# Kernel tuning notes

Hardware: AMD Instinct MI355X
Metric: run time of the kernel (lower is better)

Reference implementation:

```python
import jax, jax.numpy as jnp
import numpy as np

B, S, DM, H, DFF, NL = 4, 1024, 512, 8, 2048, 2
D = DM // H
EPS = 1e-9


def setup_inputs() -> dict:
    key = jax.random.key(0)
    ks = jax.random.split(key, 16)
    x = jax.random.normal(ks[0], (B, S, DM), jnp.float32)
    # padding-style mask: 1.0 where attention is blocked
    pad = (jax.random.uniform(ks[1], (B, S)) < 0.1).astype(jnp.float32)
    mask = jnp.maximum(pad[:, :, None], pad[:, None, :])  # [B,S,S]
    protok = jax.random.randint(ks[2], (B, S), 0, 21).astype(jnp.int32)

    def w(k, fan_in, fan_out):
        lim = np.sqrt(6.0 / (fan_in + fan_out)).astype(np.float32)
        return jax.random.uniform(k, (fan_in, fan_out), jnp.float32, -lim, lim)

    return {
        "x": x, "mask": mask, "protok": protok,
        "wq": w(ks[3], DM, DM), "bq": jnp.zeros((DM,), jnp.float32),
        "wk": w(ks[4], DM, DM), "bk": jnp.zeros((DM,), jnp.float32),
        "wv": w(ks[5], DM, DM), "bv": jnp.zeros((DM,), jnp.float32),
        "wo": w(ks[6], DM, DM), "bo": jnp.zeros((DM,), jnp.float32),
        "w1": w(ks[7], DM, DFF), "b1": jnp.zeros((DFF,), jnp.float32),
        "w2": w(ks[8], DFF, DM), "b2": jnp.zeros((DM,), jnp.float32),
        "ln1_g": jnp.ones((DM,), jnp.float32), "ln1_b": jnp.zeros((DM,), jnp.float32),
        "ln2_g": jnp.ones((DM,), jnp.float32), "ln2_b": jnp.zeros((DM,), jnp.float32),
        "layer_num": NL,
    }


def _layernorm(y, g, b):
    m = jnp.mean(y, axis=-1, keepdims=True)
    v = jnp.mean(jnp.square(y - m), axis=-1, keepdims=True)
    return (y - m) * jax.lax.rsqrt(v + EPS) * g + b


def reference(x, mask, protok, wq, bq, wk, bk, wv, bv, wo, bo,
              w1, b1, w2, b2, ln1_g, ln1_b, ln2_g, ln2_b, layer_num):
    b, s, dm = x.shape
    # count_nonzero(protok[0:1,:]) rescale for the 2D softmax (seq == max_pro_len)
    nz = jnp.count_nonzero(protok[0]).astype(jnp.float32)
    neg = mask[:, None, :, :] * -1e9  # [B,1,S,S] broadcast over heads

    def split(t):  # [B,S,DM] -> [B,H,S,D]
        return t.reshape(b, s, H, D).transpose(0, 2, 1, 3)

    def layer(h):
        q = split(h @ wq + bq)
        k = split(h @ wk + bk)
        v = split(h @ wv + bv)
        logits = jnp.einsum('bhid,bhjd->bhij', q, k) / jnp.sqrt(jnp.float32(D))
        logits = logits + neg
        # 2D softmax jointly over axes (2,3), then rescale by nonzero-token count
        A = jax.nn.softmax(logits.reshape(b, H, s * s), axis=-1).reshape(b, H, s, s) * nz
        # faithful quirk: output = A^T @ v
        o = jnp.einsum('bhji,bhjd->bhid', A, v)
        o = o.transpose(0, 2, 1, 3).reshape(b, s, dm)
        attn_out = o @ wo + bo
        out1 = _layernorm(h + attn_out, ln1_g, ln1_b)
        ffn = jax.nn.relu(out1 @ w1 + b1) @ w2 + b2
        return _layernorm(out1 + ffn, ln2_g, ln2_b)

    # Encoders reuses one shared layer layer_num times (self.rencoder overwritten in loop)
    for _ in range(int(layer_num)):
        x = layer(x)
    return x
```

## Files before the change

kernel.cpp:

```cpp
#include <hip/hip_runtime.h>

typedef unsigned short u16;
typedef __bf16 bf16x8 __attribute__((ext_vector_type(8)));
typedef float f32x4 __attribute__((ext_vector_type(4)));
typedef unsigned int u32x4 __attribute__((ext_vector_type(4)));
typedef u16 u16x4 __attribute__((ext_vector_type(4)));

#define LOG2E 1.44269504089f
#define SOFF 16.0f

__device__ __forceinline__ f32x4 mfma16(bf16x8 a, bf16x8 b, f32x4 c) {
    return __builtin_amdgcn_mfma_f32_16x16x32_bf16(a, b, c, 0, 0, 0);
}
__device__ __forceinline__ u16 f2bf(float f) {
    union { float f; unsigned u; } x; x.f = f;
    unsigned r = x.u + 0x7FFFu + ((x.u >> 16) & 1u);
    return (u16)(r >> 16);
}
__device__ __forceinline__ float bf2f(u16 u) {
    union { unsigned u; float f; } x; x.u = ((unsigned)u) << 16;
    return x.f;
}
__device__ __forceinline__ void gload_lds16(const u16* g, u16* l) {
    __builtin_amdgcn_global_load_lds((const __attribute__((address_space(1))) unsigned int*)g,
                                     (__attribute__((address_space(3))) unsigned int*)l, 16, 0, 0);
}

__device__ __forceinline__ void transp_tile(const float* __restrict__ in, u16* __restrict__ out,
                                            int R, int C, int r0, int c0,
                                            float (*t)[33], int tid) {
    const int tx = tid & 31, ty = tid >> 5;
#pragma unroll
    for (int k = 0; k < 4; ++k) t[ty + k * 8][tx] = in[(size_t)(r0 + ty + k * 8) * C + c0 + tx];
    __syncthreads();
#pragma unroll
    for (int k = 0; k < 4; ++k) out[(size_t)(c0 + ty + k * 8) * R + r0 + tx] = f2bf(t[tx][ty + k * 8]);
}

__global__ __launch_bounds__(256) void prep_kernel(
    const float* __restrict__ x,
    const float* __restrict__ wq, const float* __restrict__ wk,
    const float* __restrict__ wv, const float* __restrict__ wo,
    const float* __restrict__ w1, const float* __restrict__ w2,
    const float* __restrict__ mask, const int* __restrict__ protok,
    u16* __restrict__ hbf, u16* __restrict__ wqT, u16* __restrict__ wkT,
    u16* __restrict__ wvT, u16* __restrict__ woT, u16* __restrict__ w1T, u16* __restrict__ w2T,
    float* __restrict__ padneg, float* __restrict__ nzf) {
    __shared__ float t[32][33];
    __shared__ int red[256];
    const int id = blockIdx.x, tid = threadIdx.x;
    if (id < 1024) {
        const int z = id >> 8, rem = id & 255;
        const float* in = z == 0 ? wq : (z == 1 ? wk : (z == 2 ? wv : wo));
        u16* out = z == 0 ? wqT : (z == 1 ? wkT : (z == 2 ? wvT : woT));
        transp_tile(in, out, 512, 512, (rem >> 4) * 32, (rem & 15) * 32, t, tid);
    } else if (id < 2048) {
        const int rem = id - 1024;
        transp_tile(w1, w1T, 512, 2048, (rem >> 6) * 32, (rem & 63) * 32, t, tid);
    } else if (id < 3072) {
        const int rem = id - 2048;
        transp_tile(w2, w2T, 2048, 512, (rem >> 4) * 32, (rem & 15) * 32, t, tid);
    } else if (id < 4096) {
        const int i = ((id - 3072) * 256 + tid) * 8;
        f32x4 a = *(const f32x4*)(x + i);
        f32x4 b = *(const f32x4*)(x + i + 4);
        u16x4 o0, o1;
#pragma unroll
        for (int k = 0; k < 4; ++k) { o0[k] = f2bf(a[k]); o1[k] = f2bf(b[k]); }
        *(u16x4*)(hbf + i) = o0;
        *(u16x4*)(hbf + i + 4) = o1;
    } else if (id == 4096) {
        for (int i = tid; i < 4096; i += 256) {
            const int b = i >> 10, s = i & 1023;
            const float m = mask[(size_t)((b << 10) + s) * 1024 + s];
            padneg[i] = (m > 0.5f) ? -1.5e9f : -SOFF;
        }
    } else {
        int c = 0;
        for (int i = tid; i < 1024; i += 256) c += (protok[i] != 0) ? 1 : 0;
        red[tid] = c;
        __syncthreads();
        for (int s = 128; s > 0; s >>= 1) {
            if (tid < s) red[tid] += red[tid + s];
            __syncthreads();
        }
        if (tid == 0) nzf[0] = (float)red[0];
    }
}

template <int BM, int BN, int MODE>
__global__ __launch_bounds__(256) void gemm_bf16(
    const u16* __restrict__ A,
    const u16* __restrict__ Bt0, const u16* __restrict__ Bt1, const u16* __restrict__ Bt2,
    const float* __restrict__ bias0, const float* __restrict__ bias1, const float* __restrict__ bias2,
    void* __restrict__ dst0, void* __restrict__ dst1, void* __restrict__ dst2,
    const int K, const int N) {
    constexpr int BK = 64;
    constexpr int WM = BM / 2, WN = BN / 2, MI = WM / 16, NI = WN / 16;
    __shared__ u16 lA[BM * BK];
    __shared__ u16 lB[BN * BK];
    const int tid = threadIdx.x;
    const int w = tid >> 6, lane = tid & 63, q = lane >> 4, ln = lane & 15;
    const int wm = w >> 1, wn = w & 1;
    const int id = blockIdx.y * gridDim.x + blockIdx.x;
    const int mper = gridDim.y >> 3;
    const int rest = id >> 3;
    const int by = (id & 7) * mper + (rest % mper);
    const int bx = rest / mper;
    const int n0 = bx * BN, m0 = by * BM;
    const int rr = lane >> 3;
    const int cs = ((lane & 7) ^ rr) * 8;

    const u16* Bt;
    const float* bias;
    int nb, sel = 0;
    if (MODE == 0) {
        sel = n0 >> 9;
        Bt = sel == 0 ? Bt0 : (sel == 1 ? Bt1 : Bt2);
        bias = sel == 0 ? bias0 : (sel == 1 ? bias1 : bias2);
        nb = n0 & 511;
    } else {
        Bt = Bt0; bias = bias0; nb = n0;
    }

    const f32x4 vzero = {0.f, 0.f, 0.f, 0.f};
    f32x4 acc[MI][NI];
#pragma unroll
    for (int i = 0; i < MI; ++i)
#pragma unroll
        for (int j = 0; j < NI; ++j) acc[i][j] = vzero;

    const int swa = ln & 7;
    for (int k0 = 0; k0 < K; k0 += BK) {
        const u16* Ag = A + (size_t)m0 * K + k0;
        const u16* Bg = Bt + (size_t)nb * K + k0;
#pragma unroll
        for (int c = 0; c < BM / 32; ++c) {
            const int r = (w * (BM / 32) + c) * 8;
            gload_lds16(Ag + (size_t)(r + rr) * K + cs, &lA[r * BK]);
        }
#pragma unroll
        for (int c = 0; c < BN / 32; ++c) {
            const int r = (w * (BN / 32) + c) * 8;
            gload_lds16(Bg + (size_t)(r + rr) * K + cs, &lB[r * BK]);
        }
        __syncthreads();
#pragma unroll
        for (int kb = 0; kb < 2; ++kb) {
            bf16x8 af[MI], bfr[NI];
#pragma unroll
            for (int mi = 0; mi < MI; ++mi)
                af[mi] = *(const bf16x8*)&lA[(wm * WM + mi * 16 + ln) * BK + ((((kb << 2) + q) ^ swa) << 3)];
#pragma unroll
            for (int ni = 0; ni < NI; ++ni)
                bfr[ni] = *(const bf16x8*)&lB[(wn * WN + ni * 16 + ln) * BK + ((((kb << 2) + q) ^ swa) << 3)];
#pragma unroll
            for (int mi = 0; mi < MI; ++mi)
#pragma unroll
                for (int ni = 0; ni < NI; ++ni) acc[mi][ni] = mfma16(af[mi], bfr[ni], acc[mi][ni]);
        }
        __syncthreads();
    }

    const float scl = (MODE == 0 && sel == 1) ? 0.125f * LOG2E : 1.0f;
#pragma unroll
    for (int mi = 0; mi < MI; ++mi) {
#pragma unroll
        for (int ni = 0; ni < NI; ++ni) {
            const int col = n0 + wn * WN + ni * 16 + ln;
            const float bv = bias[MODE == 0 ? (col & 511) : col];
#pragma unroll
            for (int r = 0; r < 4; ++r) {
                const int row = m0 + wm * WM + mi * 16 + q * 4 + r;
                const float v = (acc[mi][ni][r] + bv) * scl;
                if (MODE == 0) {
                    const int cc = col & 511, hh = cc >> 6, dd = cc & 63;
                    const int bb = row >> 10, ss = row & 1023;
                    if (sel < 2) {
                        u16* dq = (u16*)(sel == 0 ? dst0 : dst1);
                        dq[(((bb << 3) + hh) * 1024 + ss) * 64 + dd] = f2bf(v);
                    } else {
                        ((u16*)dst2)[(((bb << 3) + hh) * 64 + dd) * 1024 + ss] = f2bf(v);
                    }
                } else if (MODE == 1) {
                    ((float*)dst0)[(size_t)row * N + col] = v;
                } else {
                    ((u16*)dst0)[(size_t)row * N + col] = f2bf(fmaxf(v, 0.f));
                }
            }
        }
    }
}

__global__ __launch_bounds__(256) void gemm_wo(
    const u16* __restrict__ Ounc, const float* __restrict__ blkZ, const float* __restrict__ nzf,
    const u16* __restrict__ Bt, const float* __restrict__ bias,
    float* __restrict__ dst) {
    constexpr int BM = 64, BN = 64, BK = 64, N = 512;
    constexpr int WM = 32, WN = 32, MI = 2, NI = 2;
    __shared__ u16 lA[BM * BK];
    __shared__ u16 lB[BN * BK];
    __shared__ float facsh[8];
    const int tid = threadIdx.x;
    const int w = tid >> 6, lane = tid & 63, q = lane >> 4, ln = lane & 15;
    const int wm = w >> 1, wn = w & 1;
    const int id = blockIdx.y * gridDim.x + blockIdx.x;
    const int mper = gridDim.y >> 3;
    const int rest = id >> 3;
    const int by = (id & 7) * mper + (rest % mper);
    const int bx = rest / mper;
    const int n0 = bx * BN, m0 = by * BM;
    const int b = m0 >> 10, mi0 = m0 & 1023;
    const int rr = lane >> 3;
    const int cs = ((lane & 7) ^ rr) * 8;

    {
        const int h = tid >> 5, sub = tid & 31;
        float v = blkZ[((sub >> 3) << 8) + ((b << 3) + h) * 8 + (sub & 7)];
#pragma unroll
        for (int o = 1; o < 32; o <<= 1) v += __shfl_xor(v, o);
        if (sub == 0) facsh[h] = nzf[0] / v;
    }
    __syncthreads();

    const f32x4 vzero = {0.f, 0.f, 0.f, 0.f};
    f32x4 acc[MI][NI];
#pragma unroll
    for (int i = 0; i < MI; ++i)
#pragma unroll
        for (int j = 0; j < NI; ++j) acc[i][j] = vzero;

    const int ra = tid >> 2;
    const int dseg = (tid & 3) * 16;
    const int swa = ln & 7;
    for (int k0 = 0; k0 < 512; k0 += BK) {
        const int h = k0 >> 6;
        const float fac = facsh[h];
        {
            const size_t gi = (size_t)(((b << 3) + h) << 10) + mi0 + ra;
            float vals[16];
#pragma unroll
            for (int k = 0; k < 16; ++k) vals[k] = 0.f;
#pragma unroll
            for (int c = 0; c < 4; ++c) {
                const u16* src = Ounc + (((size_t)c) << 21) + gi * 64 + dseg;
                bf16x8 x0 = *(const bf16x8*)src;
                bf16x8 x1 = *(const bf16x8*)(src + 8);
#pragma unroll
                for (int k = 0; k < 8; ++k) { vals[k] += (float)x0[k]; vals[k + 8] += (float)x1[k]; }
            }
            u16 tmp[16];
#pragma unroll
            for (int k = 0; k < 16; ++k) tmp[k] = f2bf(vals[k] * fac);
            const int c0 = (tid & 3) * 2;
            *(u32x4*)&lA[ra * BK + ((c0 ^ (ra & 7)) << 3)] = *(u32x4*)&tmp[0];
            *(u32x4*)&lA[ra * BK + (((c0 + 1) ^ (ra & 7)) << 3)] = *(u32x4*)&tmp[8];
        }
        const u16* Bg = Bt + (size_t)n0 * 512 + k0;
#pragma unroll
        for (int c = 0; c < BN / 32; ++c) {
            const int r = (w * (BN / 32) + c) * 8;
            gload_lds16(Bg + (size_t)(r + rr) * 512 + cs, &lB[r * BK]);
        }
        __syncthreads();
#pragma unroll
        for (int kb = 0; kb < 2; ++kb) {
            bf16x8 af[MI], bfr[NI];
#pragma unroll
            for (int mi = 0; mi < MI; ++mi)
                af[mi] = *(const bf16x8*)&lA[(wm * WM + mi * 16 + ln) * BK + ((((kb << 2) + q) ^ swa) << 3)];
#pragma unroll
            for (int ni = 0; ni < NI; ++ni)
                bfr[ni] = *(const bf16x8*)&lB[(wn * WN + ni * 16 + ln) * BK + ((((kb << 2) + q) ^ swa) << 3)];
#pragma unroll
            for (int mi = 0; mi < MI; ++mi)
#pragma unroll
                for (int ni = 0; ni < NI; ++ni) acc[mi][ni] = mfma16(af[mi], bfr[ni], acc[mi][ni]);
        }
        __syncthreads();
    }

#pragma unroll
    for (int mi = 0; mi < MI; ++mi) {
#pragma unroll
        for (int ni = 0; ni < NI; ++ni) {
            const int col = n0 + wn * WN + ni * 16 + ln;
            const float bv = bias[col];
#pragma unroll
            for (int r = 0; r < 4; ++r) {
                const int row = m0 + wm * WM + mi * 16 + q * 4 + r;
                dst[(size_t)row * N + col] = acc[mi][ni][r] + bv;
            }
        }
    }
}

#define PSTR 68
__global__ __launch_bounds__(256) void flash_kernel(
    const u16* __restrict__ Kb, const u16* __restrict__ Qb, const u16* __restrict__ VT,
    const float* __restrict__ padneg,
    u16* __restrict__ Ounc, float* __restrict__ blkZ) {
    __shared__ u16 ldsQ[64 * 64];
    __shared__ u16 ldsV[64 * 64];
    __shared__ u16 P[4][16 * PSTR];
    __shared__ float zred[4];
    const int blk = blockIdx.x, ck = blockIdx.y;
    const int ig = blk & 7, bh = blk >> 3, b = bh >> 3;
    const int i0 = ig << 7;
    const int tid = threadIdx.x;
    const int w = tid >> 6, lane = tid & 63, q = lane >> 4, ln = lane & 15;

    bf16x8 af[2][2];
    float pi[2][4];
    const float* pn = padneg + (b << 10);
#pragma unroll
    for (int it = 0; it < 2; ++it) {
        const u16* Ka = Kb + ((bh << 10) + i0 + (it << 6) + (w << 4) + ln) * 64;
        af[it][0] = *(const bf16x8*)(Ka + q * 8);
        af[it][1] = *(const bf16x8*)(Ka + 32 + q * 8);
#pragma unroll
        for (int r = 0; r < 4; ++r) pi[it][r] = pn[i0 + (it << 6) + (w << 4) + (q << 2) + r];
    }
    const u16* Qbase = Qb + (bh << 10) * 64;
    const u16* Vbase = VT + (bh << 6) * 1024;

    float lsum[2][4] = {{0.f, 0.f, 0.f, 0.f}, {0.f, 0.f, 0.f, 0.f}};
    const f32x4 vzero = {0.f, 0.f, 0.f, 0.f};
    f32x4 acc[2][4];
#pragma unroll
    for (int it = 0; it < 2; ++it)
#pragma unroll
        for (int ds = 0; ds < 4; ++ds) acc[it][ds] = vzero;
    u16* Pw = &P[w][0];

    const int srow = lane >> 3;
    const int scol = ((lane & 7) ^ srow) * 8;
    const int sw = ln & 7;
    const int half = w & 1;

    for (int js = 0; js < 4; ++js) {
        const int j0 = (ck << 8) + (js << 6);
        if (w < 2) {
            const u16* src = Qbase + (size_t)(j0 + half * 32) * 64;
#pragma unroll
            for (int c = 0; c < 4; ++c) {
                const int r = half * 32 + c * 8;
                gload_lds16(src + (size_t)(c * 8 + srow) * 64 + scol, &ldsQ[r * 64]);
            }
        } else {
            const u16* src = Vbase + (size_t)(half * 32) * 1024 + j0;
#pragma unroll
            for (int c = 0; c < 4; ++c) {
                const int r = half * 32 + c * 8;
                gload_lds16(src + (size_t)(c * 8 + srow) * 1024 + scol, &ldsV[r * 64]);
            }
        }
        __syncthreads();
#pragma unroll
        for (int it = 0; it < 2; ++it) {
#pragma unroll
            for (int jt = 0; jt < 4; ++jt) {
                const int jr = (jt << 4) + ln;
                const float pj = pn[j0 + jr];
                bf16x8 b0 = *(const bf16x8*)&ldsQ[jr * 64 + ((q ^ sw) << 3)];
                bf16x8 b1 = *(const bf16x8*)&ldsQ[jr * 64 + (((q + 4) ^ sw) << 3)];
                f32x4 c = vzero;
                c = mfma16(af[it][0], b0, c);
                c = mfma16(af[it][1], b1, c);
#pragma unroll
                for (int r = 0; r < 4; ++r) {
                    const float pe = exp2f(c[r] + fminf(pi[it][r], pj));
                    lsum[it][r] += pe;
                    Pw[((q << 2) + r) * PSTR + (jt << 4) + ln] = f2bf(pe);
                }
            }
            const bf16x8 pa0 = *(const bf16x8*)(Pw + ln * PSTR + q * 8);
            const bf16x8 pa1 = *(const bf16x8*)(Pw + ln * PSTR + 32 + q * 8);
#pragma unroll
            for (int ds = 0; ds < 4; ++ds) {
                const int vr = (ds << 4) + ln;
                bf16x8 v0 = *(const bf16x8*)&ldsV[vr * 64 + ((q ^ sw) << 3)];
                bf16x8 v1 = *(const bf16x8*)&ldsV[vr * 64 + (((q + 4) ^ sw) << 3)];
                acc[it][ds] = mfma16(pa0, v0, acc[it][ds]);
                acc[it][ds] = mfma16(pa1, v1, acc[it][ds]);
            }
        }
        __syncthreads();
    }
    u16* Oc = Ounc + ((size_t)ck << 21);
#pragma unroll
    for (int it = 0; it < 2; ++it) {
        const int t = (bh << 10) + i0 + (it << 6) + (w << 4) + (q << 2);
#pragma unroll
        for (int ds = 0; ds < 4; ++ds)
#pragma unroll
            for (int r = 0; r < 4; ++r) Oc[(size_t)(t + r) * 64 + (ds << 4) + ln] = f2bf(acc[it][ds][r]);
    }
    float s = (lsum[0][0] + lsum[0][1]) + (lsum[0][2] + lsum[0][3]) +
              (lsum[1][0] + lsum[1][1]) + (lsum[1][2] + lsum[1][3]);
#pragma unroll
    for (int o = 1; o < 64; o <<= 1) s += __shfl_xor(s, o);
    if (lane == 0) zred[w] = s;
    __syncthreads();
    if (tid == 0) blkZ[(ck << 8) + blk] = (zred[0] + zred[1]) + (zred[2] + zred[3]);
}

__global__ __launch_bounds__(256) void ln_kernel(
    const float* __restrict__ base, const float* __restrict__ delta,
    const float* __restrict__ g, const float* __restrict__ bb,
    float* __restrict__ of32, u16* __restrict__ obf) {
    const int t = blockIdx.x * 4 + (threadIdx.x >> 6);
    const int lane = threadIdx.x & 63;
    const int off = t * 512 + lane * 8;
    f32x4 a0 = *(const f32x4*)(base + off);
    f32x4 a1 = *(const f32x4*)(base + off + 4);
    f32x4 e0 = *(const f32x4*)(delta + off);
    f32x4 e1 = *(const f32x4*)(delta + off + 4);
    float v[8];
#pragma unroll
    for (int k = 0; k < 4; ++k) { v[k] = a0[k] + e0[k]; v[k + 4] = a1[k] + e1[k]; }
    float s = 0.f;
#pragma unroll
    for (int k = 0; k < 8; ++k) s += v[k];
#pragma unroll
    for (int o = 32; o > 0; o >>= 1) s += __shfl_xor(s, o);
    const float mean = s * (1.f / 512.f);
    float vs = 0.f;
#pragma unroll
    for (int k = 0; k < 8; ++k) { const float d = v[k] - mean; vs += d * d; }
#pragma unroll
    for (int o = 32; o > 0; o >>= 1) vs += __shfl_xor(vs, o);
    const float r = rsqrtf(vs * (1.f / 512.f) + 1e-9f);
    f32x4 y0, y1;
    u16x4 o0, o1;
#pragma unroll
    for (int k = 0; k < 4; ++k) {
        const int c = lane * 8 + k;
        const float ya = (v[k] - mean) * r * g[c] + bb[c];
        y0[k] = ya; o0[k] = f2bf(ya);
        const int c2 = c + 4;
        const float yb = (v[k + 4] - mean) * r * g[c2] + bb[c2];
        y1[k] = yb; o1[k] = f2bf(yb);
    }
    *(f32x4*)(of32 + off) = y0;
    *(f32x4*)(of32 + off + 4) = y1;
    *(u16x4*)(obf + off) = o0;
    *(u16x4*)(obf + off + 4) = o1;
}


extern "C" void kernel_launch(void* const* d_in, const int* in_sizes, int n_in,
                              void* d_out, int out_size, void* d_ws, size_t ws_size,
                              hipStream_t stream) {
    const float* x = (const float*)d_in[0];
    const float* mask = (const float*)d_in[1];
    const int* protok = (const int*)d_in[2];
    const float* wq = (const float*)d_in[3]; const float* bq = (const float*)d_in[4];
    const float* wk = (const float*)d_in[5]; const float* bk = (const float*)d_in[6];
    const float* wv = (const float*)d_in[7]; const float* bv = (const float*)d_in[8];
    const float* wo = (const float*)d_in[9]; const float* bo = (const float*)d_in[10];
    const float* w1 = (const float*)d_in[11]; const float* b1 = (const float*)d_in[12];
    const float* w2 = (const float*)d_in[13]; const float* b2 = (const float*)d_in[14];
    const float* ln1g = (const float*)d_in[15]; const float* ln1b = (const float*)d_in[16];
    const float* ln2g = (const float*)d_in[17]; const float* ln2b = (const float*)d_in[18];

    char* p = (char*)d_ws;
    auto take = [&](size_t bytes) -> char* {
        char* r = p;
        p += (bytes + 255) & ~(size_t)255;
        return r;
    };
    u16* wqT = (u16*)take(512 * 512 * 2);
    u16* wkT = (u16*)take(512 * 512 * 2);
    u16* wvT = (u16*)take(512 * 512 * 2);
    u16* woT = (u16*)take(512 * 512 * 2);
    u16* w1T = (u16*)take(2048 * 512 * 2);
    u16* w2T = (u16*)take(512 * 2048 * 2);
    u16* hbf = (u16*)take(4096 * 512 * 2);
    float* hf32 = (float*)take(4096 * 512 * 4);
    u16* qb = (u16*)take(32 * 1024 * 64 * 2);
    u16* kb = (u16*)take(32 * 1024 * 64 * 2);
    u16* vT = (u16*)take(32 * 64 * 1024 * 2);
    u16* Ounc = (u16*)take(4ull * 32 * 1024 * 64 * 2);
    float* blkZ = (float*)take(1024 * 4);
    float* nzf = (float*)take(256);
    float* padneg = (float*)take(4096 * 4);
    float* attn = (float*)take(4096 * 512 * 4);
    float* out1f = (float*)take(4096 * 512 * 4);
    u16* out1bf = (u16*)take(4096 * 512 * 2);
    u16* f1 = (u16*)take(4096 * 2048 * 2);
    float* ffn = attn;

    prep_kernel<<<dim3(4098), 256, 0, stream>>>(
        x, wq, wk, wv, wo, w1, w2, mask, protok,
        hbf, wqT, wkT, wvT, woT, w1T, w2T, padneg, nzf);

    const float* hin = x;
    for (int l = 0; l < 2; ++l) {
        gemm_bf16<128, 64, 0><<<dim3(24, 32), 256, 0, stream>>>(
            hbf, wqT, wkT, wvT, bq, bk, bv, qb, kb, vT, 512, 1536);
        flash_kernel<<<dim3(256, 4), 256, 0, stream>>>(kb, qb, vT, padneg, Ounc, blkZ);
        gemm_wo<<<dim3(8, 64), 256, 0, stream>>>(Ounc, blkZ, nzf, woT, bo, attn);
        ln_kernel<<<dim3(1024), 256, 0, stream>>>(hin, attn, ln1g, ln1b, out1f, out1bf);
        gemm_bf16<128, 128, 2><<<dim3(16, 32), 256, 0, stream>>>(
            out1bf, w1T, w1T, w1T, b1, b1, b1, f1, f1, f1, 512, 2048);
        gemm_bf16<64, 64, 1><<<dim3(8, 64), 256, 0, stream>>>(
            f1, w2T, w2T, w2T, b2, b2, b2, ffn, ffn, ffn, 2048, 512);
        float* hout = (l == 1) ? (float*)d_out : hf32;
        ln_kernel<<<dim3(1024), 256, 0, stream>>>(out1f, ffn, ln2g, ln2b, hout, hbf);
        hin = hf32;
    }
}
```

Before: 335.2 us.

## Double-buffer LDS tiles in GEMMs and flash kernel, halve attention split chunks

Adds ping-pong shared-memory buffers to the generic GEMM, the Wo GEMM and the flash attention kernel, so global-to-LDS loads for the next K tile are issued while MFMAs run on the current tile. The flash kernel's key split drops from 4 chunks to 2, each chunk covering 512 keys. This halves the partial-output buffer and the reduction reads in the Wo GEMM, and the blkZ reduction is adjusted to match. The trade-off is double the LDS per block, which may lower occupancy, and half as many flash blocks for the GPU.

```diff
diff --git a/kernel.cpp b/kernel.cpp
--- a/kernel.cpp
+++ b/kernel.cpp
@@ -97,8 +97,8 @@
     const int K, const int N) {
     constexpr int BK = 64;
     constexpr int WM = BM / 2, WN = BN / 2, MI = WM / 16, NI = WN / 16;
-    __shared__ u16 lA[BM * BK];
-    __shared__ u16 lB[BN * BK];
+    __shared__ u16 lA[2][BM * BK];
+    __shared__ u16 lB[2][BN * BK];
     const int tid = threadIdx.x;
     const int w = tid >> 6, lane = tid & 63, q = lane >> 4, ln = lane & 15;
     const int wm = w >> 1, wn = w & 1;
@@ -123,6 +123,21 @@
         Bt = Bt0; bias = bias0; nb = n0;
     }
 
+    auto stage = [&](int k0, int buf) {
+        const u16* Ag = A + (size_t)m0 * K + k0;
+        const u16* Bg = Bt + (size_t)nb * K + k0;
+#pragma unroll
+        for (int c = 0; c < BM / 32; ++c) {
+            const int r = (w * (BM / 32) + c) * 8;
+            gload_lds16(Ag + (size_t)(r + rr) * K + cs, &lA[buf][r * BK]);
+        }
+#pragma unroll
+        for (int c = 0; c < BN / 32; ++c) {
+            const int r = (w * (BN / 32) + c) * 8;
+            gload_lds16(Bg + (size_t)(r + rr) * K + cs, &lB[buf][r * BK]);
+        }
+    };
+
     const f32x4 vzero = {0.f, 0.f, 0.f, 0.f};
     f32x4 acc[MI][NI];
 #pragma unroll
@@ -131,29 +146,23 @@
         for (int j = 0; j < NI; ++j) acc[i][j] = vzero;
 
     const int swa = ln & 7;
-    for (int k0 = 0; k0 < K; k0 += BK) {
-        const u16* Ag = A + (size_t)m0 * K + k0;
-        const u16* Bg = Bt + (size_t)nb * K + k0;
-#pragma unroll
-        for (int c = 0; c < BM / 32; ++c) {
-            const int r = (w * (BM / 32) + c) * 8;
-            gload_lds16(Ag + (size_t)(r + rr) * K + cs, &lA[r * BK]);
-        }
-#pragma unroll
-        for (int c = 0; c < BN / 32; ++c) {
-            const int r = (w * (BN / 32) + c) * 8;
-            gload_lds16(Bg + (size_t)(r + rr) * K + cs, &lB[r * BK]);
-        }
-        __syncthreads();
+    const int nit = K >> 6;
+    stage(0, 0);
+    __syncthreads();
+    for (int i = 0; i < nit; ++i) {
+        const int cur = i & 1;
+        if (i + 1 < nit) stage((i + 1) << 6, cur ^ 1);
+        const u16* pA = lA[cur];
+        const u16* pB = lB[cur];
 #pragma unroll
         for (int kb = 0; kb < 2; ++kb) {
             bf16x8 af[MI], bfr[NI];
 #pragma unroll
             for (int mi = 0; mi < MI; ++mi)
-                af[mi] = *(const bf16x8*)&lA[(wm * WM + mi * 16 + ln) * BK + ((((kb << 2) + q) ^ swa) << 3)];
+                af[mi] = *(const bf16x8*)&pA[(wm * WM + mi * 16 + ln) * BK + ((((kb << 2) + q) ^ swa) << 3)];
 #pragma unroll
             for (int ni = 0; ni < NI; ++ni)
-                bfr[ni] = *(const bf16x8*)&lB[(wn * WN + ni * 16 + ln) * BK + ((((kb << 2) + q) ^ swa) << 3)];
+                bfr[ni] = *(const bf16x8*)&pB[(wn * WN + ni * 16 + ln) * BK + ((((kb << 2) + q) ^ swa) << 3)];
 #pragma unroll
             for (int mi = 0; mi < MI; ++mi)
 #pragma unroll
@@ -198,8 +207,8 @@
     float* __restrict__ dst) {
     constexpr int BM = 64, BN = 64, BK = 64, N = 512;
     constexpr int WM = 32, WN = 32, MI = 2, NI = 2;
-    __shared__ u16 lA[BM * BK];
-    __shared__ u16 lB[BN * BK];
+    __shared__ u16 lA[2][BM * BK];
+    __shared__ u16 lB[2][BN * BK];
     __shared__ float facsh[8];
     const int tid = threadIdx.x;
     const int w = tid >> 6, lane = tid & 63, q = lane >> 4, ln = lane & 15;
@@ -216,13 +225,47 @@
 
     {
         const int h = tid >> 5, sub = tid & 31;
-        float v = blkZ[((sub >> 3) << 8) + ((b << 3) + h) * 8 + (sub & 7)];
+        float v = (sub < 16) ? blkZ[((sub >> 3) << 8) + ((b << 3) + h) * 8 + (sub & 7)] : 0.f;
 #pragma unroll
         for (int o = 1; o < 32; o <<= 1) v += __shfl_xor(v, o);
         if (sub == 0) facsh[h] = nzf[0] / v;
     }
     __syncthreads();
 
+    const int ra = tid >> 2;
+    const int dseg = (tid & 3) * 16;
+    auto stageB = [&](int k0, int buf) {
+        const u16* Bg = Bt + (size_t)n0 * 512 + k0;
+#pragma unroll
+        for (int c = 0; c < BN / 32; ++c) {
+            const int r = (w * (BN / 32) + c) * 8;
+            gload_lds16(Bg + (size_t)(r + rr) * 512 + cs, &lB[buf][r * BK]);
+        }
+    };
+    auto synthA = [&](int k0, int buf) {
+        const int h = k0 >> 6;
+        const float fac = facsh[h];
+        const size_t gi = (size_t)(((b << 3) + h) << 10) + mi0 + ra;
+        float vals[16];
+#pragma unroll
+        for (int k = 0; k < 16; ++k) vals[k] = 0.f;
+#pragma unroll
+        for (int c = 0; c < 2; ++c) {
+            const u16* src = Ounc + (((size_t)c) << 21) + gi * 64 + dseg;
+            bf16x8 x0 = *(const bf16x8*)src;
+            bf16x8 x1 = *(const bf16x8*)(src + 8);
+#pragma unroll
+            for (int k = 0; k < 8; ++k) { vals[k] += (float)x0[k]; vals[k + 8] += (float)x1[k]; }
+        }
+        u16 tmp[16];
+#pragma unroll
+        for (int k = 0; k < 16; ++k) tmp[k] = f2bf(vals[k] * fac);
+        const int c0 = (tid & 3) * 2;
+        u16* dstl = &lA[buf][ra * BK];
+        *(u32x4*)&dstl[(c0 ^ (ra & 7)) << 3] = *(u32x4*)&tmp[0];
+        *(u32x4*)&dstl[((c0 + 1) ^ (ra & 7)) << 3] = *(u32x4*)&tmp[8];
+    };
+
     const f32x4 vzero = {0.f, 0.f, 0.f, 0.f};
     f32x4 acc[MI][NI];
 #pragma unroll
@@ -230,48 +273,24 @@
 #pragma unroll
         for (int j = 0; j < NI; ++j) acc[i][j] = vzero;
 
-    const int ra = tid >> 2;
-    const int dseg = (tid & 3) * 16;
     const int swa = ln & 7;
-    for (int k0 = 0; k0 < 512; k0 += BK) {
-        const int h = k0 >> 6;
-        const float fac = facsh[h];
-        {
-            const size_t gi = (size_t)(((b << 3) + h) << 10) + mi0 + ra;
-            float vals[16];
-#pragma unroll
-            for (int k = 0; k < 16; ++k) vals[k] = 0.f;
-#pragma unroll
-            for (int c = 0; c < 4; ++c) {
-                const u16* src = Ounc + (((size_t)c) << 21) + gi * 64 + dseg;
-                bf16x8 x0 = *(const bf16x8*)src;
-                bf16x8 x1 = *(const bf16x8*)(src + 8);
-#pragma unroll
-                for (int k = 0; k < 8; ++k) { vals[k] += (float)x0[k]; vals[k + 8] += (float)x1[k]; }
-            }
-            u16 tmp[16];
-#pragma unroll
-            for (int k = 0; k < 16; ++k) tmp[k] = f2bf(vals[k] * fac);
-            const int c0 = (tid & 3) * 2;
-            *(u32x4*)&lA[ra * BK + ((c0 ^ (ra & 7)) << 3)] = *(u32x4*)&tmp[0];
-            *(u32x4*)&lA[ra * BK + (((c0 + 1) ^ (ra & 7)) << 3)] = *(u32x4*)&tmp[8];
-        }
-        const u16* Bg = Bt + (size_t)n0 * 512 + k0;
-#pragma unroll
-        for (int c = 0; c < BN / 32; ++c) {
-            const int r = (w * (BN / 32) + c) * 8;
-            gload_lds16(Bg + (size_t)(r + rr) * 512 + cs, &lB[r * BK]);
-        }
-        __syncthreads();
+    stageB(0, 0);
+    synthA(0, 0);
+    __syncthreads();
+    for (int i = 0; i < 8; ++i) {
+        const int cur = i & 1;
+        if (i < 7) { stageB((i + 1) << 6, cur ^ 1); synthA((i + 1) << 6, cur ^ 1); }
+        const u16* pA = lA[cur];
+        const u16* pB = lB[cur];
 #pragma unroll
         for (int kb = 0; kb < 2; ++kb) {
             bf16x8 af[MI], bfr[NI];
 #pragma unroll
             for (int mi = 0; mi < MI; ++mi)
-                af[mi] = *(const bf16x8*)&lA[(wm * WM + mi * 16 + ln) * BK + ((((kb << 2) + q) ^ swa) << 3)];
+                af[mi] = *(const bf16x8*)&pA[(wm * WM + mi * 16 + ln) * BK + ((((kb << 2) + q) ^ swa) << 3)];
 #pragma unroll
             for (int ni = 0; ni < NI; ++ni)
-                bfr[ni] = *(const bf16x8*)&lB[(wn * WN + ni * 16 + ln) * BK + ((((kb << 2) + q) ^ swa) << 3)];
+                bfr[ni] = *(const bf16x8*)&pB[(wn * WN + ni * 16 + ln) * BK + ((((kb << 2) + q) ^ swa) << 3)];
 #pragma unroll
             for (int mi = 0; mi < MI; ++mi)
 #pragma unroll
@@ -300,8 +319,8 @@
     const u16* __restrict__ Kb, const u16* __restrict__ Qb, const u16* __restrict__ VT,
     const float* __restrict__ padneg,
     u16* __restrict__ Ounc, float* __restrict__ blkZ) {
-    __shared__ u16 ldsQ[64 * 64];
-    __shared__ u16 ldsV[64 * 64];
+    __shared__ u16 ldsQ[2][64 * 64];
+    __shared__ u16 ldsV[2][64 * 64];
     __shared__ u16 P[4][16 * PSTR];
     __shared__ float zred[4];
     const int blk = blockIdx.x, ck = blockIdx.y;
@@ -324,46 +343,53 @@
     const u16* Qbase = Qb + (bh << 10) * 64;
     const u16* Vbase = VT + (bh << 6) * 1024;
 
-    float lsum[2][4] = {{0.f, 0.f, 0.f, 0.f}, {0.f, 0.f, 0.f, 0.f}};
-    const f32x4 vzero = {0.f, 0.f, 0.f, 0.f};
-    f32x4 acc[2][4];
-#pragma unroll
-    for (int it = 0; it < 2; ++it)
-#pragma unroll
-        for (int ds = 0; ds < 4; ++ds) acc[it][ds] = vzero;
-    u16* Pw = &P[w][0];
-
     const int srow = lane >> 3;
     const int scol = ((lane & 7) ^ srow) * 8;
     const int sw = ln & 7;
     const int half = w & 1;
-
-    for (int js = 0; js < 4; ++js) {
-        const int j0 = (ck << 8) + (js << 6);
+    auto stage = [&](int j0, int buf) {
         if (w < 2) {
             const u16* src = Qbase + (size_t)(j0 + half * 32) * 64;
 #pragma unroll
             for (int c = 0; c < 4; ++c) {
                 const int r = half * 32 + c * 8;
-                gload_lds16(src + (size_t)(c * 8 + srow) * 64 + scol, &ldsQ[r * 64]);
+                gload_lds16(src + (size_t)(c * 8 + srow) * 64 + scol, &ldsQ[buf][r * 64]);
             }
         } else {
             const u16* src = Vbase + (size_t)(half * 32) * 1024 + j0;
 #pragma unroll
             for (int c = 0; c < 4; ++c) {
                 const int r = half * 32 + c * 8;
-                gload_lds16(src + (size_t)(c * 8 + srow) * 1024 + scol, &ldsV[r * 64]);
+                gload_lds16(src + (size_t)(c * 8 + srow) * 1024 + scol, &ldsV[buf][r * 64]);
             }
         }
-        __syncthreads();
+    };
+
+    float lsum[2][4] = {{0.f, 0.f, 0.f, 0.f}, {0.f, 0.f, 0.f, 0.f}};
+    const f32x4 vzero = {0.f, 0.f, 0.f, 0.f};
+    f32x4 acc[2][4];
+#pragma unroll
+    for (int it = 0; it < 2; ++it)
+#pragma unroll
+        for (int ds = 0; ds < 4; ++ds) acc[it][ds] = vzero;
+    u16* Pw = &P[w][0];
+
+    stage(ck << 9, 0);
+    __syncthreads();
+    for (int js = 0; js < 8; ++js) {
+        const int j0 = (ck << 9) + (js << 6);
+        const int cur = js & 1;
+        if (js < 7) stage(j0 + 64, cur ^ 1);
+        const u16* pQ = ldsQ[cur];
+        const u16* pV = ldsV[cur];
 #pragma unroll
         for (int it = 0; it < 2; ++it) {
 #pragma unroll
             for (int jt = 0; jt < 4; ++jt) {
                 const int jr = (jt << 4) + ln;
                 const float pj = pn[j0 + jr];
-                bf16x8 b0 = *(const bf16x8*)&ldsQ[jr * 64 + ((q ^ sw) << 3)];
-                bf16x8 b1 = *(const bf16x8*)&ldsQ[jr * 64 + (((q + 4) ^ sw) << 3)];
+                bf16x8 b0 = *(const bf16x8*)&pQ[jr * 64 + ((q ^ sw) << 3)];
+                bf16x8 b1 = *(const bf16x8*)&pQ[jr * 64 + (((q + 4) ^ sw) << 3)];
                 f32x4 c = vzero;
                 c = mfma16(af[it][0], b0, c);
                 c = mfma16(af[it][1], b1, c);
@@ -379,8 +405,8 @@
 #pragma unroll
             for (int ds = 0; ds < 4; ++ds) {
                 const int vr = (ds << 4) + ln;
-                bf16x8 v0 = *(const bf16x8*)&ldsV[vr * 64 + ((q ^ sw) << 3)];
-                bf16x8 v1 = *(const bf16x8*)&ldsV[vr * 64 + (((q + 4) ^ sw) << 3)];
+                bf16x8 v0 = *(const bf16x8*)&pV[vr * 64 + ((q ^ sw) << 3)];
+                bf16x8 v1 = *(const bf16x8*)&pV[vr * 64 + (((q + 4) ^ sw) << 3)];
                 acc[it][ds] = mfma16(pa0, v0, acc[it][ds]);
                 acc[it][ds] = mfma16(pa1, v1, acc[it][ds]);
             }
@@ -481,8 +507,8 @@
     u16* qb = (u16*)take(32 * 1024 * 64 * 2);
     u16* kb = (u16*)take(32 * 1024 * 64 * 2);
     u16* vT = (u16*)take(32 * 64 * 1024 * 2);
-    u16* Ounc = (u16*)take(4ull * 32 * 1024 * 64 * 2);
-    float* blkZ = (float*)take(1024 * 4);
+    u16* Ounc = (u16*)take(2ull * 32 * 1024 * 64 * 2);
+    float* blkZ = (float*)take(512 * 4);
     float* nzf = (float*)take(256);
     float* padneg = (float*)take(4096 * 4);
     float* attn = (float*)take(4096 * 512 * 4);
@@ -499,7 +525,7 @@
     for (int l = 0; l < 2; ++l) {
         gemm_bf16<128, 64, 0><<<dim3(24, 32), 256, 0, stream>>>(
             hbf, wqT, wkT, wvT, bq, bk, bv, qb, kb, vT, 512, 1536);
-        flash_kernel<<<dim3(256, 4), 256, 0, stream>>>(kb, qb, vT, padneg, Ounc, blkZ);
+        flash_kernel<<<dim3(256, 2), 256, 0, stream>>>(kb, qb, vT, padneg, Ounc, blkZ);
         gemm_wo<<<dim3(8, 64), 256, 0, stream>>>(Ounc, blkZ, nzf, woT, bo, attn);
         ln_kernel<<<dim3(1024), 256, 0, stream>>>(hin, attn, ln1g, ln1b, out1f, out1bf);
         gemm_bf16<128, 128, 2><<<dim3(16, 32), 256, 0, stream>>>(
```

Measured after the change: 339.6 us. About the same (+1.3%).
